# Kernel optimization log

Measured on AMD Instinct MI355X. Metric: run time of the kernel, lower is better.

Reference implementation:

```python
import jax, jax.numpy as jnp
import numpy as np

B, N, E = 4, 512, 128
NODE_F, EDGE_F, DYN_F, L = 16, 8, 6, 3
TOT_F = NODE_F + DYN_F  # 22


def setup_inputs() -> dict:
    key = jax.random.key(0)
    ks = jax.random.split(key, 20)
    s = 0.05
    return {
        "node_features": jax.random.normal(ks[0], (B, N, NODE_F), jnp.float32),
        "edge_features": jax.random.normal(ks[1], (B, N, N, EDGE_F), jnp.float32),
        "W": jax.random.normal(ks[2], (B, N, N), jnp.float32),
        "assigned": jax.random.randint(ks[3], (B, N), 0, 2) > 0,
        "open_group": jax.random.randint(ks[4], (B, N), 0, 2) > 0,
        "action_mask": jax.random.randint(ks[5], (B, N), 0, 2) > 0,
        "build_limit": jax.random.uniform(ks[6], (B, 3), jnp.float32, 0.5, 2.0),
        "open_group_size": jax.random.uniform(ks[7], (B, 3), jnp.float32, 0.0, 2.0),
        "node_embed_w": jax.random.normal(ks[8], (TOT_F, E), jnp.float32) * s,
        "node_embed_b": jnp.zeros((E,), jnp.float32),
        "mp_node_w": jax.random.normal(ks[9], (L, E, E), jnp.float32) * s,
        "mp_edge_w": jax.random.normal(ks[10], (L, EDGE_F, E), jnp.float32) * s,
        "mp_weight_w": jax.random.normal(ks[11], (L, E), jnp.float32) * s,
        "mp_out_w": jax.random.normal(ks[12], (L, E, E), jnp.float32) * s,
        "mp_out_b": jnp.zeros((L, E), jnp.float32),
        "context_w": jax.random.normal(ks[13], (E, E), jnp.float32) * s,
        "key_w": jax.random.normal(ks[14], (E, E), jnp.float32) * s,
        "logit_bias": jnp.zeros((1,), jnp.float32),
    }


def _policy_logits(node_features, edge_features, W, build_limit, open_group_size,
                   node_embed_w, node_embed_b, mp_node_w, mp_edge_w, mp_weight_w,
                   mp_out_w, mp_out_b, context_w, key_w, logit_bias,
                   assigned, open_group, action_mask):
    # --- dynamic node features: [B,N,6] ---
    ratio = open_group_size / jnp.maximum(build_limit, 1e-6)  # [B,3]
    dyn = jnp.concatenate([
        assigned.astype(jnp.float32)[..., None],
        open_group.astype(jnp.float32)[..., None],
        action_mask.astype(jnp.float32)[..., None],
        jnp.broadcast_to(ratio[:, None, :], (node_features.shape[0], node_features.shape[1], 3)),
    ], axis=-1)
    x = jnp.concatenate([node_features, dyn], axis=-1)  # [B,N,22]
    h = x @ node_embed_w + node_embed_b  # [B,N,E]

    # --- edge-aware message passing, residual per layer ---
    for l in range(L):
        hi = h @ mp_node_w[l]  # [B,N,E]
        ej = jnp.einsum('bijf,fe->bije', edge_features, mp_edge_w[l])  # [B,N,N,E]
        wij = W[..., None] * mp_weight_w[l]  # [B,N,N,E]
        msg = jnp.tanh(hi[:, :, None, :] + ej + wij)  # [B,N,N,E]
        agg = msg.mean(axis=2)  # [B,N,E]
        h = h + agg @ mp_out_w[l] + mp_out_b[l]

    # --- context attention logits ---
    og = open_group.astype(jnp.float32)
    has_open = jnp.any(open_group, axis=-1, keepdims=True)  # [B,1]
    denom = jnp.maximum(og.sum(axis=-1, keepdims=True), 1.0)  # [B,1]
    group_mean = (h * og[..., None]).sum(axis=1) / denom  # [B,E]
    sep_emb = h[:, 0, :]
    context = jnp.where(has_open, group_mean, sep_emb)  # [B,E]
    query = context @ context_w  # [B,E]
    keys = h @ key_w  # [B,N,E]
    logits = jnp.einsum('be,bne->bn', query, keys) / jnp.sqrt(jnp.float32(h.shape[-1]))
    logits = logits + logit_bias[0]
    logits = jnp.where(action_mask, logits, -1e9)
    return logits


def reference(node_features, edge_features, W, assigned, open_group, action_mask,
              build_limit, open_group_size, node_embed_w, node_embed_b,
              mp_node_w, mp_edge_w, mp_weight_w, mp_out_w, mp_out_b,
              context_w, key_w, logit_bias):
    return _policy_logits(node_features, edge_features, W, build_limit, open_group_size,
                          node_embed_w, node_embed_b, mp_node_w, mp_edge_w, mp_weight_w,
                          mp_out_w, mp_out_b, context_w, key_w, logit_bias,
                          assigned, open_group, action_mask)
```

## Files before the change

### kernel.cpp

```cpp
#include <hip/hip_runtime.h>
#include <math.h>

#define BB 4
#define NN 512
#define EE 128
#define NODE_F 16
#define EDGE_F 8
#define LL 3

typedef __attribute__((ext_vector_type(8))) short bf16x8;
typedef __attribute__((ext_vector_type(4))) float f32x4;

__device__ __forceinline__ ushort bf_hi(float x) {
    uint u = __float_as_uint(x);
    return (ushort)((u + 0x7fffu + ((u >> 16) & 1u)) >> 16);
}
__device__ __forceinline__ float bf_f(ushort h) {
    return __uint_as_float(((uint)h) << 16);
}

__global__ __launch_bounds__(512) void k_rows(
    const float* __restrict__ nf,
    const float* __restrict__ ef,
    const float* __restrict__ W,
    const int*   __restrict__ assigned,
    const int*   __restrict__ open_group,
    const int*   __restrict__ action_mask,
    const float* __restrict__ build_limit,
    const float* __restrict__ open_group_size,
    const float* __restrict__ embed_w,
    const float* __restrict__ embed_b,
    const float* __restrict__ node_w,
    const float* __restrict__ edge_w,
    const float* __restrict__ weight_w,
    const float* __restrict__ out_w,
    const float* __restrict__ out_b,
    float* __restrict__ hout)
{
    const int i   = blockIdx.x;
    const int b   = blockIdx.y;
    const int t   = threadIdx.x;
    const int l   = t & 63;
    const int w   = t >> 6;
    const int e   = t & 127;
    const int ks  = t >> 7;
    const int row = b * NN + i;

    __shared__ bf16x8 afr[32 * 64];
    __shared__ float hsh[EE];
    __shared__ float hipart[4][EE];
    __shared__ float opart[4][EE];
    __shared__ float aggfin[EE];
    __shared__ float xsh[24];

    if (t < NODE_F) {
        xsh[t] = nf[row * NODE_F + t];
    } else if (t == 16) {
        xsh[16] = assigned[row] ? 1.0f : 0.0f;
    } else if (t == 17) {
        xsh[17] = open_group[row] ? 1.0f : 0.0f;
    } else if (t == 18) {
        xsh[18] = action_mask[row] ? 1.0f : 0.0f;
    } else if (t < 22) {
        int k = t - 19;
        xsh[t] = open_group_size[b * 3 + k] / fmaxf(build_limit[b * 3 + k], 1e-6f);
    }

    {
        const float* efr = ef + (size_t)row * NN * EDGE_F;
        const float* Wr  = W + (size_t)row * NN;
        #pragma unroll
        for (int q = 0; q < 4; ++q) {
            const int eid = t + 512 * q;
            const int ll  = eid & 63;
            const int jt  = eid >> 6;
            const int g   = ll >> 4;
            const int jj  = jt * 16 + (ll & 15);
            bf16x8 frag;
            if (g < 3) {
                const float4 a = *(const float4*)&efr[jj * 8];
                const float4 c4 = *(const float4*)&efr[jj * 8 + 4];
                float v[8] = {a.x, a.y, a.z, a.w, c4.x, c4.y, c4.z, c4.w};
                if (g < 2) {
                    #pragma unroll
                    for (int m = 0; m < 8; ++m) frag[m] = (short)bf_hi(v[m]);
                } else {
                    #pragma unroll
                    for (int m = 0; m < 8; ++m) {
                        ushort h = bf_hi(v[m]);
                        frag[m] = (short)bf_hi(v[m] - bf_f(h));
                    }
                }
            } else {
                float wv = Wr[jj];
                ushort h = bf_hi(wv);
                ushort lo = bf_hi(wv - bf_f(h));
                frag = (bf16x8){(short)h, (short)h, (short)lo, 0, 0, 0, 0, 0};
            }
            afr[eid] = frag;
        }
    }
    __syncthreads();

    if (t < EE) {
        float h0 = embed_b[t];
        #pragma unroll
        for (int k = 0; k < 22; ++k)
            h0 = fmaf(xsh[k], embed_w[k * EE + t], h0);
        hsh[t] = h0;
    }

    const float c  = 2.8853900817779268f;
    const int  le  = l & 15;
    const int  g   = l >> 4;
    const int  eN  = w * 16 + le;

    for (int lay = 0; lay < LL; ++lay) {
        __syncthreads();

        {
            const float* nw = node_w + lay * EE * EE + ks * 32 * EE + e;
            float hp = 0.0f;
            #pragma unroll 8
            for (int k = 0; k < 32; ++k)
                hp = fmaf(hsh[ks * 32 + k], nw[k * EE], hp);
            hipart[ks][e] = hp;
        }

        bf16x8 bfrag;
        if (g == 3) {
            float x = c * weight_w[lay * EE + eN];
            ushort h = bf_hi(x);
            ushort lo = bf_hi(x - bf_f(h));
            bfrag = (bf16x8){(short)h, (short)lo, (short)h, 0, 0, 0, 0, 0};
        } else {
            const float* ewp = edge_w + lay * EDGE_F * EE + eN;
            if (g == 1) {
                #pragma unroll
                for (int m = 0; m < 8; ++m) {
                    float x = c * ewp[m * EE];
                    ushort h = bf_hi(x);
                    bfrag[m] = (short)bf_hi(x - bf_f(h));
                }
            } else {
                #pragma unroll
                for (int m = 0; m < 8; ++m)
                    bfrag[m] = (short)bf_hi(c * ewp[m * EE]);
            }
        }
        __syncthreads();

        const float hq = c * ((hipart[0][eN] + hipart[1][eN])
                            + (hipart[2][eN] + hipart[3][eN]));
        const f32x4 cin = {hq, hq, hq, hq};

        float rsum = 0.0f;
        #pragma unroll 4
        for (int jt = 0; jt < 32; ++jt) {
            bf16x8 a = afr[jt * 64 + l];
            f32x4 acc = __builtin_amdgcn_mfma_f32_16x16x32_bf16(a, bfrag, cin, 0, 0, 0);
            float A0 = __builtin_amdgcn_exp2f(fminf(acc[0], 30.0f)) + 1.0f;
            float A1 = __builtin_amdgcn_exp2f(fminf(acc[1], 30.0f)) + 1.0f;
            float A2 = __builtin_amdgcn_exp2f(fminf(acc[2], 30.0f)) + 1.0f;
            float A3 = __builtin_amdgcn_exp2f(fminf(acc[3], 30.0f)) + 1.0f;
            float P01 = A0 * A1, S01 = A0 + A1;
            float P23 = A2 * A3, S23 = A2 + A3;
            float Nn = fmaf(P01, S23, S01 * P23);
            float Dd = P01 * P23;
            rsum = fmaf(Nn, __builtin_amdgcn_rcpf(Dd), rsum);
        }
        float s = rsum;
        s += __shfl_xor(s, 16);
        s += __shfl_xor(s, 32);
        if (l < 16)
            aggfin[w * 16 + le] = 1.0f - s * (1.0f / 256.0f);
        __syncthreads();

        {
            const float* ow = out_w + lay * EE * EE + ks * 32 * EE + e;
            float op = 0.0f;
            #pragma unroll 8
            for (int k = 0; k < 32; ++k)
                op = fmaf(aggfin[ks * 32 + k], ow[k * EE], op);
            opart[ks][e] = op;
        }
        __syncthreads();

        if (t < EE) {
            hsh[t] = hsh[t] + out_b[lay * EE + t]
                   + (opart[0][t] + opart[1][t]) + (opart[2][t] + opart[3][t]);
        }
    }

    __syncthreads();
    if (t < EE) hout[(size_t)row * EE + t] = hsh[t];
}

__global__ __launch_bounds__(1024) void k_tail(
    const float* __restrict__ hbuf,
    const int*   __restrict__ open_group,
    const float* __restrict__ context_w,
    const float* __restrict__ key_w,
    const int*   __restrict__ action_mask,
    const float* __restrict__ logit_bias,
    float* __restrict__ out)
{
    const int b = blockIdx.x;
    const int t = threadIdx.x;
    const int e = t & 127;
    const int s = t >> 7;

    __shared__ float gmsh[8][EE];
    __shared__ float cntsh[8];
    __shared__ float csh[EE];
    __shared__ float qsh[EE];
    __shared__ float qksh[EE];

    const float* hb = hbuf + (size_t)b * NN * EE;

    float gm = 0.0f, cnt = 0.0f;
    const int n0 = s * 64;
    #pragma unroll 4
    for (int u = 0; u < 64; ++u) {
        const int n = n0 + u;
        const float m = (float)open_group[b * NN + n];
        gm = fmaf(m, hb[(size_t)n * EE + e], gm);
        cnt += m;
    }
    gmsh[s][e] = gm;
    if (e == 0) cntsh[s] = cnt;
    __syncthreads();

    if (s == 0) {
        float ca = 0.0f, ga = 0.0f;
        #pragma unroll
        for (int u = 0; u < 8; ++u) { ca += cntsh[u]; ga += gmsh[u][e]; }
        csh[e] = (ca > 0.0f) ? (ga / fmaxf(ca, 1.0f)) : hb[e];
    }
    __syncthreads();

    if (s == 0) {
        float q = 0.0f;
        #pragma unroll 8
        for (int k = 0; k < EE; ++k)
            q = fmaf(csh[k], context_w[k * EE + e], q);
        qsh[e] = q;
    }
    __syncthreads();

    if (s == 0) {
        float acc = 0.0f;
        const float* kr = key_w + e * EE;
        #pragma unroll 8
        for (int k = 0; k < EE; ++k)
            acc = fmaf(kr[k], qsh[k], acc);
        qksh[e] = acc;
    }
    __syncthreads();

    const int wid  = t >> 6;
    const int lane = t & 63;
    const float lb = logit_bias[0];

    for (int r = wid; r < NN; r += 16) {
        const float* hr = hb + (size_t)r * EE;
        float p = hr[lane] * qksh[lane] + hr[lane + 64] * qksh[lane + 64];
        #pragma unroll
        for (int off = 32; off; off >>= 1)
            p += __shfl_down(p, off);
        if (lane == 0) {
            float v = fmaf(p, 0.08838834764831845f, lb);
            out[b * NN + r] = action_mask[b * NN + r] ? v : -1000000000.0f;
        }
    }
}

extern "C" void kernel_launch(void* const* d_in, const int* in_sizes, int n_in,
                              void* d_out, int out_size, void* d_ws, size_t ws_size,
                              hipStream_t stream) {
    const float* nf         = (const float*)d_in[0];
    const float* ef         = (const float*)d_in[1];
    const float* W          = (const float*)d_in[2];
    const int*   assigned   = (const int*)d_in[3];
    const int*   open_group = (const int*)d_in[4];
    const int*   action_mask= (const int*)d_in[5];
    const float* build_limit= (const float*)d_in[6];
    const float* og_size    = (const float*)d_in[7];
    const float* embed_w    = (const float*)d_in[8];
    const float* embed_b    = (const float*)d_in[9];
    const float* node_w     = (const float*)d_in[10];
    const float* edge_w     = (const float*)d_in[11];
    const float* weight_w   = (const float*)d_in[12];
    const float* out_w      = (const float*)d_in[13];
    const float* out_b      = (const float*)d_in[14];
    const float* context_w  = (const float*)d_in[15];
    const float* key_w      = (const float*)d_in[16];
    const float* logit_bias = (const float*)d_in[17];

    float* hbuf = (float*)d_ws;

    dim3 grid_rows(NN, BB, 1);
    k_rows<<<grid_rows, 512, 0, stream>>>(nf, ef, W, assigned, open_group,
        action_mask, build_limit, og_size, embed_w, embed_b, node_w, edge_w,
        weight_w, out_w, out_b, hbuf);

    k_tail<<<BB, 1024, 0, stream>>>(hbuf, open_group, context_w, key_w,
        action_mask, logit_bias, (float*)d_out);
}
```

Baseline: 248.8 us.

## Batch weight loads, simplify sigmoid reduction, split tail into context and logits kernels

The node and output matvec loops now load 16 weights into registers before the FMAs, so more global loads are in flight at once. The sigmoid accumulation changes from the paired product/rational form to a per-element exp2 plus reciprocal with four independent accumulators, and it drops the clamp at 30. The tail kernel is split into a 4-block context/query kernel and a 64-block logits kernel, so the per-row dot products are spread across more CUs. This adds a kernel launch and a global round trip for qk, and without the clamp, large exponents now rely on exp2 overflowing to infinity and the reciprocal going to zero.

```diff
diff --git a/kernel.cpp b/kernel.cpp
--- a/kernel.cpp
+++ b/kernel.cpp
@@ -121,9 +121,16 @@
         {
             const float* nw = node_w + lay * EE * EE + ks * 32 * EE + e;
             float hp = 0.0f;
-            #pragma unroll 8
-            for (int k = 0; k < 32; ++k)
-                hp = fmaf(hsh[ks * 32 + k], nw[k * EE], hp);
+            #pragma unroll
+            for (int kk = 0; kk < 2; ++kk) {
+                float wreg[16];
+                #pragma unroll
+                for (int k2 = 0; k2 < 16; ++k2)
+                    wreg[k2] = nw[(kk * 16 + k2) * EE];
+                #pragma unroll
+                for (int k2 = 0; k2 < 16; ++k2)
+                    hp = fmaf(hsh[ks * 32 + kk * 16 + k2], wreg[k2], hp);
+            }
             hipart[ks][e] = hp;
         }
 
@@ -154,22 +161,18 @@
                             + (hipart[2][eN] + hipart[3][eN]));
         const f32x4 cin = {hq, hq, hq, hq};
 
-        float rsum = 0.0f;
+        f32x4 rsum = {0.0f, 0.0f, 0.0f, 0.0f};
         #pragma unroll 4
         for (int jt = 0; jt < 32; ++jt) {
             bf16x8 a = afr[jt * 64 + l];
             f32x4 acc = __builtin_amdgcn_mfma_f32_16x16x32_bf16(a, bfrag, cin, 0, 0, 0);
-            float A0 = __builtin_amdgcn_exp2f(fminf(acc[0], 30.0f)) + 1.0f;
-            float A1 = __builtin_amdgcn_exp2f(fminf(acc[1], 30.0f)) + 1.0f;
-            float A2 = __builtin_amdgcn_exp2f(fminf(acc[2], 30.0f)) + 1.0f;
-            float A3 = __builtin_amdgcn_exp2f(fminf(acc[3], 30.0f)) + 1.0f;
-            float P01 = A0 * A1, S01 = A0 + A1;
-            float P23 = A2 * A3, S23 = A2 + A3;
-            float Nn = fmaf(P01, S23, S01 * P23);
-            float Dd = P01 * P23;
-            rsum = fmaf(Nn, __builtin_amdgcn_rcpf(Dd), rsum);
-        }
-        float s = rsum;
+            #pragma unroll
+            for (int r = 0; r < 4; ++r) {
+                float ex = __builtin_amdgcn_exp2f(acc[r]);
+                rsum[r] += __builtin_amdgcn_rcpf(ex + 1.0f);
+            }
+        }
+        float s = (rsum[0] + rsum[1]) + (rsum[2] + rsum[3]);
         s += __shfl_xor(s, 16);
         s += __shfl_xor(s, 32);
         if (l < 16)
@@ -179,9 +182,16 @@
         {
             const float* ow = out_w + lay * EE * EE + ks * 32 * EE + e;
             float op = 0.0f;
-            #pragma unroll 8
-            for (int k = 0; k < 32; ++k)
-                op = fmaf(aggfin[ks * 32 + k], ow[k * EE], op);
+            #pragma unroll
+            for (int kk = 0; kk < 2; ++kk) {
+                float wreg[16];
+                #pragma unroll
+                for (int k2 = 0; k2 < 16; ++k2)
+                    wreg[k2] = ow[(kk * 16 + k2) * EE];
+                #pragma unroll
+                for (int k2 = 0; k2 < 16; ++k2)
+                    op = fmaf(aggfin[ks * 32 + kk * 16 + k2], wreg[k2], op);
+            }
             opart[ks][e] = op;
         }
         __syncthreads();
@@ -196,14 +206,12 @@
     if (t < EE) hout[(size_t)row * EE + t] = hsh[t];
 }
 
-__global__ __launch_bounds__(1024) void k_tail(
+__global__ __launch_bounds__(1024) void k_ctx(
     const float* __restrict__ hbuf,
     const int*   __restrict__ open_group,
     const float* __restrict__ context_w,
     const float* __restrict__ key_w,
-    const int*   __restrict__ action_mask,
-    const float* __restrict__ logit_bias,
-    float* __restrict__ out)
+    float* __restrict__ qk)
 {
     const int b = blockIdx.x;
     const int t = threadIdx.x;
@@ -214,13 +222,12 @@
     __shared__ float cntsh[8];
     __shared__ float csh[EE];
     __shared__ float qsh[EE];
-    __shared__ float qksh[EE];
 
     const float* hb = hbuf + (size_t)b * NN * EE;
 
     float gm = 0.0f, cnt = 0.0f;
     const int n0 = s * 64;
-    #pragma unroll 4
+    #pragma unroll 8
     for (int u = 0; u < 64; ++u) {
         const int n = n0 + u;
         const float m = (float)open_group[b * NN + n];
@@ -241,9 +248,16 @@
 
     if (s == 0) {
         float q = 0.0f;
-        #pragma unroll 8
-        for (int k = 0; k < EE; ++k)
-            q = fmaf(csh[k], context_w[k * EE + e], q);
+        #pragma unroll
+        for (int kk = 0; kk < 8; ++kk) {
+            float wreg[16];
+            #pragma unroll
+            for (int k2 = 0; k2 < 16; ++k2)
+                wreg[k2] = context_w[(kk * 16 + k2) * EE + e];
+            #pragma unroll
+            for (int k2 = 0; k2 < 16; ++k2)
+                q = fmaf(csh[kk * 16 + k2], wreg[k2], q);
+        }
         qsh[e] = q;
     }
     __syncthreads();
@@ -251,20 +265,43 @@
     if (s == 0) {
         float acc = 0.0f;
         const float* kr = key_w + e * EE;
-        #pragma unroll 8
-        for (int k = 0; k < EE; ++k)
-            acc = fmaf(kr[k], qsh[k], acc);
-        qksh[e] = acc;
-    }
-    __syncthreads();
-
-    const int wid  = t >> 6;
-    const int lane = t & 63;
+        #pragma unroll
+        for (int kk = 0; kk < 8; ++kk) {
+            float wreg[16];
+            #pragma unroll
+            for (int k2 = 0; k2 < 16; ++k2)
+                wreg[k2] = kr[kk * 16 + k2];
+            #pragma unroll
+            for (int k2 = 0; k2 < 16; ++k2)
+                acc = fmaf(wreg[k2], qsh[kk * 16 + k2], acc);
+        }
+        qk[b * EE + e] = acc;
+    }
+}
+
+__global__ __launch_bounds__(512) void k_logits(
+    const float* __restrict__ hbuf,
+    const float* __restrict__ qk,
+    const int*   __restrict__ action_mask,
+    const float* __restrict__ logit_bias,
+    float* __restrict__ out)
+{
+    const int b    = blockIdx.y;
+    const int base = blockIdx.x * 32;
+    const int wid  = threadIdx.x >> 6;
+    const int lane = threadIdx.x & 63;
+
+    const float* hb = hbuf + (size_t)b * NN * EE;
+    const float* qb = qk + b * EE;
+    const float q0 = qb[lane];
+    const float q1 = qb[lane + 64];
     const float lb = logit_bias[0];
 
-    for (int r = wid; r < NN; r += 16) {
+    #pragma unroll
+    for (int u = 0; u < 4; ++u) {
+        const int r = base + wid * 4 + u;
         const float* hr = hb + (size_t)r * EE;
-        float p = hr[lane] * qksh[lane] + hr[lane + 64] * qksh[lane + 64];
+        float p = hr[lane] * q0 + hr[lane + 64] * q1;
         #pragma unroll
         for (int off = 32; off; off >>= 1)
             p += __shfl_down(p, off);
@@ -298,12 +335,16 @@
     const float* logit_bias = (const float*)d_in[17];
 
     float* hbuf = (float*)d_ws;
+    float* qk   = hbuf + (size_t)BB * NN * EE;
 
     dim3 grid_rows(NN, BB, 1);
     k_rows<<<grid_rows, 512, 0, stream>>>(nf, ef, W, assigned, open_group,
         action_mask, build_limit, og_size, embed_w, embed_b, node_w, edge_w,
         weight_w, out_w, out_b, hbuf);
 
-    k_tail<<<BB, 1024, 0, stream>>>(hbuf, open_group, context_w, key_w,
-        action_mask, logit_bias, (float*)d_out);
-}
+    k_ctx<<<BB, 1024, 0, stream>>>(hbuf, open_group, context_w, key_w, qk);
+
+    dim3 grid_log(16, BB, 1);
+    k_logits<<<grid_log, 512, 0, stream>>>(hbuf, qk, action_mask, logit_bias,
+        (float*)d_out);
+}
```

Result: faster. 231.7 us (-6.9%).
